# Kernel tuning notes

Measured on AMD Instinct MI355X. Metric: run time of the kernel, lower is better.

## Reference

```python
import jax, jax.numpy as jnp
import numpy as np

jax.config.update("jax_enable_x64", True)  # original uses .double() for the partition function

B, L, NS = 32768, 16, 1024  # batch, n_labels, n_legal_states


def setup_inputs() -> dict:
    key = jax.random.key(0)
    kf, ky, ks = jax.random.split(key, 3)
    f = jax.random.normal(kf, (B, L), dtype=jnp.float32)
    y = jax.random.uniform(ky, (B, L), dtype=jnp.float32)  # soft labels in [0,1]
    S = jax.random.randint(ks, (NS, L), 0, 2).astype(jnp.int32)  # binary legal-state matrix
    return {"f": f, "y": y, "S": S}


def _focal_fidelity(p, g, gamma=2.0, alpha=0.75, eps=1e-8):
    p = p.reshape(-1)
    g = g.reshape(-1)
    fidelity = jnp.sqrt(p * g + eps) + jnp.sqrt((1.0 - p) * (1.0 - g) + eps)
    p_t = p * g + (1.0 - p) * (1.0 - g)
    alpha_t = alpha * g + (1.0 - alpha) * (1.0 - g)
    loss = (1.0 - fidelity) * alpha_t * (1.0 - p_t) ** gamma
    return jnp.mean(loss)


def reference(f, y, S):
    Sd = S.astype(jnp.float64)                      # [NS, L]
    potential = Sd @ f.T.astype(jnp.float64)        # [NS, B]
    max_sf = jnp.max(potential, axis=0)             # [B]
    J = jnp.exp(potential - max_sf)                 # [NS, B]
    z = jnp.sum(J, axis=0)                          # [B]
    # fused batched segment-reduce over states: indicator.T @ J replaces the per-column loop
    num = (S > 0).astype(jnp.float64).T @ J         # [L, B]
    pMargin = (num / z).T.astype(jnp.float32)       # [B, L]
    all_loss = _focal_fidelity(pMargin, y)
    return all_loss, pMargin
```

## Files before the change

### kernel.cpp

```cpp
#include <hip/hip_runtime.h>
#include <math.h>

#define LBL 16
#define B_TOTAL 32768
#define WAVES 8
#define BLOCK_THREADS (WAVES * 64)
#define COLS_PER_BLOCK 64
#define GRID_BLOCKS (B_TOTAL / COLS_PER_BLOCK)

#define SCM_WOFF 8192
#define SCM_STRIDE 516
#define LDS_WORDS (SCM_WOFF + LBL * SCM_STRIDE)

typedef __attribute__((ext_vector_type(8))) short bf16x8;
typedef __attribute__((ext_vector_type(4))) float f32x4;

#define LOG2E 1.4426950408889634f

#if __has_builtin(__builtin_amdgcn_exp2f)
#define EXP2F __builtin_amdgcn_exp2f
#else
#define EXP2F exp2f
#endif

static __device__ __forceinline__ unsigned short bf16_rne(float x) {
    union { float f; unsigned u; } v; v.f = x;
    unsigned r = v.u + 0x7FFFu + ((v.u >> 16) & 1u);
    return (unsigned short)(r >> 16);
}
static __device__ __forceinline__ float bf16_to_f(unsigned short h) {
    union { unsigned u; float f; } v; v.u = ((unsigned)h) << 16;
    return v.f;
}
static __device__ __forceinline__ unsigned cvt_pk_bf16(float lo, float hi) {
    unsigned r;
    asm("v_cvt_pk_bf16_f32 %0, %1, %2" : "=v"(r) : "v"(lo), "v"(hi));
    return r;
}

#define PKB(p, q) ((((p) > 0) ? 0x3F80u : 0u) | (((q) > 0) ? 0x3F800000u : 0u))

__global__ __launch_bounds__(BLOCK_THREADS, 4) void plm_mfma6(
    const float* __restrict__ f, const float* __restrict__ y,
    const int* __restrict__ S, float* __restrict__ out,
    float* __restrict__ block_loss)
{
    __shared__ __align__(16) unsigned SH[LDS_WORDS];
    unsigned short* U16 = (unsigned short*)SH;
    float* part = (float*)SH;
    float* wls  = (float*)(SH + 2560);

    const int tid = threadIdx.x;

    {
        const int s0 = tid * 2;
        int b0[16], b1[16];
        {
            const int4* sp = (const int4*)(S + (size_t)s0 * LBL);
            int4 a = sp[0], bq = sp[1], cq = sp[2], dq = sp[3];
            b0[0]=a.x;  b0[1]=a.y;  b0[2]=a.z;  b0[3]=a.w;
            b0[4]=bq.x; b0[5]=bq.y; b0[6]=bq.z; b0[7]=bq.w;
            b0[8]=cq.x; b0[9]=cq.y; b0[10]=cq.z;b0[11]=cq.w;
            b0[12]=dq.x;b0[13]=dq.y;b0[14]=dq.z;b0[15]=dq.w;
        }
        {
            const int4* sp = (const int4*)(S + (size_t)(s0 + 1) * LBL);
            int4 a = sp[0], bq = sp[1], cq = sp[2], dq = sp[3];
            b1[0]=a.x;  b1[1]=a.y;  b1[2]=a.z;  b1[3]=a.w;
            b1[4]=bq.x; b1[5]=bq.y; b1[6]=bq.z; b1[7]=bq.w;
            b1[8]=cq.x; b1[9]=cq.y; b1[10]=cq.z;b1[11]=cq.w;
            b1[12]=dq.x;b1[13]=dq.y;b1[14]=dq.z;b1[15]=dq.w;
        }
        const int half_s = s0 >> 9, tt = (s0 >> 5) & 15, o = s0 & 31;
        const int q = (o >> 2) & 1;
        const int x = ((o >> 4) & 1) * 8 + ((o >> 3) & 1) * 4 + (o & 3);
        const int slot = half_s * 512 + tt * 32 + q * 16 + x;
        unsigned short* Urow = U16 + slot * 16;
        uint4 ua = { PKB(b0[0],b0[1]),  PKB(b0[2],b0[3]),  PKB(b0[4],b0[5]),  PKB(b0[6],b0[7]) };
        uint4 ub = { PKB(b0[8],b0[9]),  PKB(b0[10],b0[11]),PKB(b0[12],b0[13]),PKB(b0[14],b0[15]) };
        uint4 uc = { PKB(b1[0],b1[1]),  PKB(b1[2],b1[3]),  PKB(b1[4],b1[5]),  PKB(b1[6],b1[7]) };
        uint4 ud = { PKB(b1[8],b1[9]),  PKB(b1[10],b1[11]),PKB(b1[12],b1[13]),PKB(b1[14],b1[15]) };
        *(uint4*)&Urow[0]  = ua;
        *(uint4*)&Urow[8]  = ub;
        *(uint4*)&Urow[16] = uc;
        *(uint4*)&Urow[24] = ud;
#pragma unroll
        for (int l = 0; l < 16; ++l) {
            unsigned v = (((b0[l] > 0) ? 0x3F80u : 0u)) | (((b1[l] > 0) ? 0x3F800000u : 0u));
            SH[SCM_WOFF + l * SCM_STRIDE + ((unsigned)tid ^ ((unsigned)(l & 3) << 2))] = v;
        }
    }
    __syncthreads();

    const int w = tid >> 6, lane = tid & 63;
    const int c = lane & 15;
    const int g = lane >> 4;
    const int cg = w & 3;
    const int half = w >> 2;
    const int b = blockIdx.x * COLS_PER_BLOCK + cg * LBL + c;
    const int h = g & 1;
    const int hilo = g >> 1;

    const float4* fr = (const float4*)(f + (size_t)b * LBL + h * 8);
    float4 x0 = fr[0], x1 = fr[1];
    float xs[8] = { x0.x, x0.y, x0.z, x0.w, x1.x, x1.y, x1.z, x1.w };
#pragma unroll
    for (int j = 0; j < 8; ++j) xs[j] *= LOG2E;

    float up = 0.f;
#pragma unroll
    for (int j = 0; j < 8; ++j) up += fmaxf(xs[j], 0.f);
    const float U2 = up + __shfl_xor(up, 16);
    const float nUb = -U2;
    const f32x4 cin = { nUb, nUb, nUb, nUb };

    union { unsigned short s[8]; bf16x8 v; } b1u;
#pragma unroll
    for (int j = 0; j < 8; ++j) {
        unsigned short hb = bf16_rne(xs[j]);
        unsigned short lb = bf16_rne(xs[j] - bf16_to_f(hb));
        b1u.s[j] = (unsigned short)(hilo ? lb : hb);
    }
    const bf16x8 b1f = b1u.v;

    const unsigned gc = (unsigned)(g ^ (c & 3));
    const char* baseA  = (const char*)SH + half * 16384 + 32 * c + 16 * h;
    const char* baseS2 = (const char*)SH + SCM_WOFF * 4 + 2064 * c + 1024 * half + 16 * gc;

    f32x4 cacc = 0.0f;
    float zacc = 0.f;

#pragma unroll
    for (int t = 0; t < 16; ++t) {
        const char* pa = baseA + t * 1024;
        bf16x8 A0 = *(const bf16x8*)(pa);
        bf16x8 A1 = *(const bf16x8*)(pa + 512);
        bf16x8 a2 = *(const bf16x8*)(baseS2 + t * 64);

        f32x4 pot0 = __builtin_amdgcn_mfma_f32_16x16x32_bf16(A0, b1f, cin, 0, 0, 0);
        f32x4 pot1 = __builtin_amdgcn_mfma_f32_16x16x32_bf16(A1, b1f, cin, 0, 0, 0);

        float e0 = EXP2F(pot0[0]), e1 = EXP2F(pot0[1]);
        float e2 = EXP2F(pot0[2]), e3 = EXP2F(pot0[3]);
        float e4 = EXP2F(pot1[0]), e5 = EXP2F(pot1[1]);
        float e6 = EXP2F(pot1[2]), e7 = EXP2F(pot1[3]);
        zacc += ((e0 + e1) + (e2 + e3)) + ((e4 + e5) + (e6 + e7));

        union { unsigned u[4]; bf16x8 v; } b2;
        b2.u[0] = cvt_pk_bf16(e0, e1);
        b2.u[1] = cvt_pk_bf16(e2, e3);
        b2.u[2] = cvt_pk_bf16(e4, e5);
        b2.u[3] = cvt_pk_bf16(e6, e7);

        cacc = __builtin_amdgcn_mfma_f32_16x16x32_bf16(a2, b2.v, cacc, 0, 0, 0);
    }

    __syncthreads();
    *(f32x4*)&part[(w * 16 + c) * 20 + 4 * g] = cacc;
    part[(w * 16 + c) * 20 + 16 + g] = zacc;
    __syncthreads();

    {
        const int cg2 = tid >> 7;
        const int c2  = (tid >> 3) & 15;
        const int lp  = tid & 7;
        const int w0 = cg2, w1 = cg2 + 4;
        const int bg = blockIdx.x * COLS_PER_BLOCK + cg2 * LBL + c2;

        float z = 0.f;
#pragma unroll
        for (int gg = 0; gg < 4; ++gg)
            z += part[(w0 * 16 + c2) * 20 + 16 + gg] + part[(w1 * 16 + c2) * 20 + 16 + gg];
        const float invz = 1.0f / z;

        const float2 yv = *(const float2*)(y + (size_t)bg * LBL + 2 * lp);
        float yr[2] = { yv.x, yv.y };
        float* prow = out + 1 + (size_t)bg * LBL + 2 * lp;

        float ls = 0.f;
#pragma unroll
        for (int r2 = 0; r2 < 2; ++r2) {
            const int l = 2 * lp + r2;
            float num = part[(w0 * 16 + c2) * 20 + l] + part[(w1 * 16 + c2) * 20 + l];
            float p = num * invz;
            prow[r2] = p;
            float gv = yr[r2];
            float fid = sqrtf(fmaf(p, gv, 1e-8f)) + sqrtf(fmaf(1.f - p, 1.f - gv, 1e-8f));
            float pt = fmaf(p, gv, (1.f - p) * (1.f - gv));
            float at = fmaf(0.75f, gv, 0.25f * (1.f - gv));
            float om = 1.f - pt;
            ls += (1.f - fid) * at * om * om;
        }
#pragma unroll
        for (int off = 32; off; off >>= 1) ls += __shfl_down(ls, off);
        if (lane == 0) wls[w] = ls;
    }
    __syncthreads();
    if (tid == 0) {
        float t = 0.f;
#pragma unroll
        for (int i = 0; i < WAVES; ++i) t += wls[i];
        block_loss[blockIdx.x] = t;
    }
}

__global__ __launch_bounds__(256) void plm_reduce(
    const float* __restrict__ block_loss, int n, float* __restrict__ out)
{
    __shared__ float wsum[4];
    float s = 0.f;
    for (int i = threadIdx.x; i < n; i += 256) s += block_loss[i];
#pragma unroll
    for (int off = 32; off; off >>= 1) s += __shfl_down(s, off);
    const int wave = threadIdx.x >> 6;
    if ((threadIdx.x & 63) == 0) wsum[wave] = s;
    __syncthreads();
    if (threadIdx.x == 0) {
        float t = (wsum[0] + wsum[1]) + (wsum[2] + wsum[3]);
        out[0] = t * (1.0f / ((float)B_TOTAL * (float)LBL));
    }
}

extern "C" void kernel_launch(void* const* d_in, const int* in_sizes, int n_in,
                              void* d_out, int out_size, void* d_ws, size_t ws_size,
                              hipStream_t stream) {
    const float* f = (const float*)d_in[0];
    const float* y = (const float*)d_in[1];
    const int*   S = (const int*)d_in[2];
    float* out = (float*)d_out;
    float* bl  = (float*)d_ws;

    plm_mfma6<<<GRID_BLOCKS, BLOCK_THREADS, 0, stream>>>(f, y, S, out, bl);
    plm_reduce<<<1, 256, 0, stream>>>(bl, GRID_BLOCKS, out);
}
```

Before: 18.00 us.

## Fuse final loss reduction via last-block atomic counter and MFMA partition sum

Removes the separate reduce kernel launch: each block publishes its partial loss, bumps a global counter, and the last-arriving block sums all partials. The per-lane partition-function sum is replaced by an extra MFMA with an all-ones A operand. The part/wls buffers get their own LDS arrays, so the barrier before writing them is dropped. This costs extra LDS, an extra MFMA per iteration, and partition sums taken from bf16-rounded exponentials. The counter relies on the modulo-512 wrap, assuming it starts at a multiple of 512.

```diff
diff --git a/kernel.cpp b/kernel.cpp
--- a/kernel.cpp
+++ b/kernel.cpp
@@ -40,15 +40,16 @@
 
 #define PKB(p, q) ((((p) > 0) ? 0x3F80u : 0u) | (((q) > 0) ? 0x3F800000u : 0u))
 
-__global__ __launch_bounds__(BLOCK_THREADS, 4) void plm_mfma6(
+__global__ __launch_bounds__(BLOCK_THREADS, 4) void plm_mfma7(
     const float* __restrict__ f, const float* __restrict__ y,
     const int* __restrict__ S, float* __restrict__ out,
-    float* __restrict__ block_loss)
+    float* __restrict__ block_loss, unsigned* __restrict__ cnt)
 {
     __shared__ __align__(16) unsigned SH[LDS_WORDS];
+    __shared__ __align__(16) float part[WAVES * 16 * 20];
+    __shared__ float wls[WAVES];
+    __shared__ int flag;
     unsigned short* U16 = (unsigned short*)SH;
-    float* part = (float*)SH;
-    float* wls  = (float*)(SH + 2560);
 
     const int tid = threadIdx.x;
 
@@ -123,12 +124,16 @@
     }
     const bf16x8 b1f = b1u.v;
 
+    union { unsigned u[4]; bf16x8 v; } onesA;
+    onesA.u[0] = 0x3F803F80u; onesA.u[1] = 0x3F803F80u;
+    onesA.u[2] = 0x3F803F80u; onesA.u[3] = 0x3F803F80u;
+
     const unsigned gc = (unsigned)(g ^ (c & 3));
     const char* baseA  = (const char*)SH + half * 16384 + 32 * c + 16 * h;
     const char* baseS2 = (const char*)SH + SCM_WOFF * 4 + 2064 * c + 1024 * half + 16 * gc;
 
     f32x4 cacc = 0.0f;
-    float zacc = 0.f;
+    f32x4 zvec = 0.0f;
 
 #pragma unroll
     for (int t = 0; t < 16; ++t) {
@@ -144,7 +149,6 @@
         float e2 = EXP2F(pot0[2]), e3 = EXP2F(pot0[3]);
         float e4 = EXP2F(pot1[0]), e5 = EXP2F(pot1[1]);
         float e6 = EXP2F(pot1[2]), e7 = EXP2F(pot1[3]);
-        zacc += ((e0 + e1) + (e2 + e3)) + ((e4 + e5) + (e6 + e7));
 
         union { unsigned u[4]; bf16x8 v; } b2;
         b2.u[0] = cvt_pk_bf16(e0, e1);
@@ -153,11 +157,11 @@
         b2.u[3] = cvt_pk_bf16(e6, e7);
 
         cacc = __builtin_amdgcn_mfma_f32_16x16x32_bf16(a2, b2.v, cacc, 0, 0, 0);
-    }
-
-    __syncthreads();
+        zvec = __builtin_amdgcn_mfma_f32_16x16x32_bf16(onesA.v, b2.v, zvec, 0, 0, 0);
+    }
+
     *(f32x4*)&part[(w * 16 + c) * 20 + 4 * g] = cacc;
-    part[(w * 16 + c) * 20 + 16 + g] = zacc;
+    part[(w * 16 + c) * 20 + 16 + g] = zvec[0];
     __syncthreads();
 
     {
@@ -167,10 +171,7 @@
         const int w0 = cg2, w1 = cg2 + 4;
         const int bg = blockIdx.x * COLS_PER_BLOCK + cg2 * LBL + c2;
 
-        float z = 0.f;
-#pragma unroll
-        for (int gg = 0; gg < 4; ++gg)
-            z += part[(w0 * 16 + c2) * 20 + 16 + gg] + part[(w1 * 16 + c2) * 20 + 16 + gg];
+        const float z = part[(w0 * 16 + c2) * 20 + 16] + part[(w1 * 16 + c2) * 20 + 16];
         const float invz = 1.0f / z;
 
         const float2 yv = *(const float2*)(y + (size_t)bg * LBL + 2 * lp);
@@ -196,28 +197,23 @@
         if (lane == 0) wls[w] = ls;
     }
     __syncthreads();
+
     if (tid == 0) {
         float t = 0.f;
 #pragma unroll
         for (int i = 0; i < WAVES; ++i) t += wls[i];
-        block_loss[blockIdx.x] = t;
-    }
-}
-
-__global__ __launch_bounds__(256) void plm_reduce(
-    const float* __restrict__ block_loss, int n, float* __restrict__ out)
-{
-    __shared__ float wsum[4];
-    float s = 0.f;
-    for (int i = threadIdx.x; i < n; i += 256) s += block_loss[i];
-#pragma unroll
-    for (int off = 32; off; off >>= 1) s += __shfl_down(s, off);
-    const int wave = threadIdx.x >> 6;
-    if ((threadIdx.x & 63) == 0) wsum[wave] = s;
-    __syncthreads();
-    if (threadIdx.x == 0) {
-        float t = (wsum[0] + wsum[1]) + (wsum[2] + wsum[3]);
-        out[0] = t * (1.0f / ((float)B_TOTAL * (float)LBL));
+        __hip_atomic_store(&block_loss[blockIdx.x], t, __ATOMIC_RELEASE, __HIP_MEMORY_SCOPE_AGENT);
+        unsigned old = __hip_atomic_fetch_add(cnt, 1u, __ATOMIC_ACQ_REL, __HIP_MEMORY_SCOPE_AGENT);
+        flag = ((old & 511u) == 511u) ? 1 : 0;
+    }
+    __syncthreads();
+    if (flag && tid < 64) {
+        float s = 0.f;
+        for (int i = tid; i < GRID_BLOCKS; i += 64)
+            s += __hip_atomic_load(&block_loss[i], __ATOMIC_RELAXED, __HIP_MEMORY_SCOPE_AGENT);
+#pragma unroll
+        for (int off = 32; off; off >>= 1) s += __shfl_down(s, off);
+        if (tid == 0) out[0] = s * (1.0f / ((float)B_TOTAL * (float)LBL));
     }
 }
 
@@ -229,7 +225,7 @@
     const int*   S = (const int*)d_in[2];
     float* out = (float*)d_out;
     float* bl  = (float*)d_ws;
-
-    plm_mfma6<<<GRID_BLOCKS, BLOCK_THREADS, 0, stream>>>(f, y, S, out, bl);
-    plm_reduce<<<1, 256, 0, stream>>>(bl, GRID_BLOCKS, out);
-}
+    unsigned* cnt = (unsigned*)((char*)d_ws + GRID_BLOCKS * sizeof(float));
+
+    plm_mfma7<<<GRID_BLOCKS, BLOCK_THREADS, 0, stream>>>(f, y, S, out, bl, cnt);
+}
```

Result: slower. 29.35 us (+63.0%).
